# Optimization experiments

Measured on AMD Instinct MI355X. Metric: run time of the kernel, lower is better.

Reference implementation:

```python
import jax, jax.numpy as jnp
import numpy as np

NUM_HEAD = 12
D_MODEL = 768
SEQ_LEN = 4096
D_K = D_MODEL // NUM_HEAD
NEG = -1e9  # matches masked_fill(-1000000000.0)


def setup_inputs() -> dict:
    key = jax.random.key(0)
    ks = jax.random.split(key, 9)
    s = 1.0 / np.sqrt(D_MODEL)
    inp = {
        "x": jax.random.normal(ks[0], (1, SEQ_LEN, D_MODEL), jnp.float32),
        "Wq": jax.random.normal(ks[1], (D_MODEL, D_MODEL), jnp.float32) * s,
        "bq": jax.random.normal(ks[2], (D_MODEL,), jnp.float32) * 0.01,
        "Wk": jax.random.normal(ks[3], (D_MODEL, D_MODEL), jnp.float32) * s,
        "bk": jax.random.normal(ks[4], (D_MODEL,), jnp.float32) * 0.01,
        "Wv": jax.random.normal(ks[5], (D_MODEL, D_MODEL), jnp.float32) * s,
        "bv": jax.random.normal(ks[6], (D_MODEL,), jnp.float32) * 0.01,
        "Wo": jax.random.normal(ks[7], (D_MODEL, D_MODEL), jnp.float32) * s,
        "bo": jax.random.normal(ks[8], (D_MODEL,), jnp.float32) * 0.01,
    }
    return inp


def reference(x, Wq, bq, Wk, bk, Wv, bv, Wo, bo):
    # x: [B, S, D]. nn.Linear computes x @ W.T + b.
    B, S, D = x.shape

    def proj(W, b):
        y = jnp.einsum("bsd,ed->bse", x, W) + b
        # [B, S, H, d_k] -> [B, H, S, d_k]
        return y.reshape(B, S, NUM_HEAD, D_K).transpose(0, 2, 1, 3)

    q = proj(Wq, bq)
    k = proj(Wk, bk)
    v = proj(Wv, bv)

    scores = jnp.einsum("bhqd,bhkd->bhqk", q, k) / jnp.sqrt(
        jnp.asarray(D_K, x.dtype)
    )
    # causal (subsequent) mask: position q attends to k <= q
    causal = jnp.tril(jnp.ones((S, S), bool))
    scores = jnp.where(causal[None, None], scores, jnp.asarray(NEG, x.dtype))
    p_attn = jax.nn.softmax(scores, axis=-1)  # dropout is identity in eval
    ctx = jnp.einsum("bhqk,bhkd->bhqd", p_attn, v)
    ctx = ctx.transpose(0, 2, 1, 3).reshape(B, S, D)
    return jnp.einsum("bsd,ed->bse", ctx, Wo) + bo
```

## Files before the change

### kernel.cpp

```cpp
#include <hip/hip_runtime.h>

#define SEQ 4096
#define DM  768
#define NH  12
#define DK  64

typedef __bf16 bf16_t;
typedef bf16_t bf16x8 __attribute__((ext_vector_type(8)));
typedef bf16_t bf16x4 __attribute__((ext_vector_type(4)));
typedef float  f32x4  __attribute__((ext_vector_type(4)));
typedef short  s16x4  __attribute__((ext_vector_type(4)));

#define LOG2E 1.44269504088896340736f
#define SM_C  16.0f

static __device__ inline f32x4 mfma16x16x16_bf16(bf16x4 a, bf16x4 b, f32x4 c) {
#if __has_builtin(__builtin_amdgcn_mfma_f32_16x16x16_bf16)
    return __builtin_amdgcn_mfma_f32_16x16x16_bf16(a, b, c, 0, 0, 0);
#else
    return __builtin_amdgcn_mfma_f32_16x16x16bf16_1k(
        __builtin_bit_cast(s16x4, a), __builtin_bit_cast(s16x4, b), c, 0, 0, 0);
#endif
}

static __device__ __forceinline__ void gl_lds16(const bf16_t* g, bf16_t* l) {
    __builtin_amdgcn_global_load_lds(
        (const __attribute__((address_space(1))) void*)g,
        (__attribute__((address_space(3))) void*)l, 16, 0, 0);
}

__global__ __launch_bounds__(256) void cvt_zero(
    const float* __restrict__ x,  const float* __restrict__ Wq,
    const float* __restrict__ Wk, const float* __restrict__ Wv,
    const float* __restrict__ Wo,
    bf16_t* __restrict__ xb, bf16_t* __restrict__ Wb,
    float* __restrict__ zf )
{
    const int NXV  = SEQ * DM / 4;
    const int NWV  = DM * DM / 4;
    const int NCVT = NXV + 4 * NWV;
    int i4 = blockIdx.x * 256 + threadIdx.x;
    if (i4 < NCVT) {
        const float* src; bf16_t* dst; int off;
        if (i4 < NXV) { src = x; dst = xb; off = i4; }
        else {
            int j = i4 - NXV;
            int w = j / NWV, jj = j - w * NWV;
            src = (w == 0) ? Wq : (w == 1) ? Wk : (w == 2) ? Wv : Wo;
            dst = Wb + (size_t)w * DM * DM;
            off = jj;
        }
        float4 v = *(const float4*)&src[(size_t)off * 4];
        bf16x4 t;
        t[0] = (bf16_t)v.x; t[1] = (bf16_t)v.y;
        t[2] = (bf16_t)v.z; t[3] = (bf16_t)v.w;
        *(bf16x4*)&dst[(size_t)off * 4] = t;
    } else {
        int j = i4 - NCVT;
        *(float4*)&zf[(size_t)j * 4] = (float4){0.f, 0.f, 0.f, 0.f};
    }
}

__global__ __launch_bounds__(256) void gemm_qkv2(
    const bf16_t* __restrict__ A, const bf16_t* __restrict__ Wb,
    const float* __restrict__ bq, const float* __restrict__ bk,
    const float* __restrict__ bv,
    bf16_t* __restrict__ Qb, bf16_t* __restrict__ Kb, bf16_t* __restrict__ Vbt)
{
    const int z = blockIdx.z;
    const bf16_t* W = Wb + (size_t)z * DM * DM;
    const float* bias = (z == 0) ? bq : (z == 1) ? bk : bv;

    __shared__ bf16_t As[128][64];
    __shared__ bf16_t Bs[128][64];

    const int tid  = threadIdx.x;
    const int wave = tid >> 6;
    const int lane = tid & 63;
    const int wm   = wave & 1, wn = wave >> 1;
    const int lrow = lane & 15;
    const int quad = lane >> 4;
    const int row0 = blockIdx.x * 128;
    const int col0 = blockIdx.y * 128;

    const int srow   = lane >> 3;
    const int schunk = (lane & 7) ^ srow;
    const int swz    = lrow & 7;

    f32x4 acc[4][4];
    #pragma unroll
    for (int i = 0; i < 4; i++)
        #pragma unroll
        for (int j = 0; j < 4; j++)
            acc[i][j] = (f32x4){0.f, 0.f, 0.f, 0.f};

    for (int k0 = 0; k0 < DM; k0 += 64) {
        __syncthreads();
        #pragma unroll
        for (int u = 0; u < 4; u++) {
            int R0 = wave * 32 + u * 8;
            gl_lds16(&A[(size_t)(row0 + R0 + srow) * DM + k0 + schunk * 8],
                     &As[R0][0]);
            gl_lds16(&W[(size_t)(col0 + R0 + srow) * DM + k0 + schunk * 8],
                     &Bs[R0][0]);
        }
        __syncthreads();

        #pragma unroll
        for (int s = 0; s < 2; s++) {
            bf16x8 af[4], bfr[4];
            #pragma unroll
            for (int mt = 0; mt < 4; mt++)
                af[mt] = *(const bf16x8*)
                    &As[wm * 64 + mt * 16 + lrow][(((s << 2) | quad) ^ swz) * 8];
            #pragma unroll
            for (int nt = 0; nt < 4; nt++)
                bfr[nt] = *(const bf16x8*)
                    &Bs[wn * 64 + nt * 16 + lrow][(((s << 2) | quad) ^ swz) * 8];
            #pragma unroll
            for (int mt = 0; mt < 4; mt++)
                #pragma unroll
                for (int nt = 0; nt < 4; nt++)
                    acc[mt][nt] = __builtin_amdgcn_mfma_f32_16x16x32_bf16(
                        af[mt], bfr[nt], acc[mt][nt], 0, 0, 0);
        }
    }

    if (z == 2) {
        #pragma unroll
        for (int nt = 0; nt < 4; nt++) {
            int col = col0 + wn * 64 + nt * 16 + lrow;
            float bvv = bias[col];
            #pragma unroll
            for (int mt = 0; mt < 4; mt++) {
                int row = row0 + wm * 64 + mt * 16 + quad * 4;
                bf16x4 t;
                #pragma unroll
                for (int r = 0; r < 4; r++) t[r] = (bf16_t)(acc[mt][nt][r] + bvv);
                *(bf16x4*)&Vbt[(size_t)col * SEQ + row] = t;
            }
        }
    } else {
        bf16_t* Cout = (z == 0) ? Qb : Kb;
        float scale = (z == 1) ? 0.125f : 1.0f;
        #pragma unroll
        for (int nt = 0; nt < 4; nt++) {
            int col = col0 + wn * 64 + nt * 16 + lrow;
            float bvv = bias[col];
            #pragma unroll
            for (int mt = 0; mt < 4; mt++) {
                #pragma unroll
                for (int r = 0; r < 4; r++) {
                    int row = row0 + wm * 64 + mt * 16 + quad * 4 + r;
                    Cout[(size_t)row * DM + col] =
                        (bf16_t)((acc[mt][nt][r] + bvv) * scale);
                }
            }
        }
    }
}

__global__ __launch_bounds__(256) void gemm_out2(
    const bf16_t* __restrict__ A, const bf16_t* __restrict__ W,
    const float* __restrict__ bias, float* __restrict__ C)
{
    __shared__ bf16_t As[128][64];
    __shared__ bf16_t Bs[64][64];

    const int tid  = threadIdx.x;
    const int wave = tid >> 6;
    const int lane = tid & 63;
    const int wm   = wave & 1, wn = wave >> 1;
    const int lrow = lane & 15;
    const int quad = lane >> 4;
    const int row0 = blockIdx.x * 128;
    const int col0 = blockIdx.y * 64;

    const int srow   = lane >> 3;
    const int schunk = (lane & 7) ^ srow;
    const int swz    = lrow & 7;

    f32x4 acc[4][2];
    #pragma unroll
    for (int i = 0; i < 4; i++)
        #pragma unroll
        for (int j = 0; j < 2; j++)
            acc[i][j] = (f32x4){0.f, 0.f, 0.f, 0.f};

    for (int k0 = 0; k0 < DM; k0 += 64) {
        __syncthreads();
        #pragma unroll
        for (int u = 0; u < 4; u++) {
            int R0 = wave * 32 + u * 8;
            gl_lds16(&A[(size_t)(row0 + R0 + srow) * DM + k0 + schunk * 8],
                     &As[R0][0]);
        }
        #pragma unroll
        for (int u = 0; u < 2; u++) {
            int R0 = wave * 16 + u * 8;
            gl_lds16(&W[(size_t)(col0 + R0 + srow) * DM + k0 + schunk * 8],
                     &Bs[R0][0]);
        }
        __syncthreads();

        #pragma unroll
        for (int s = 0; s < 2; s++) {
            bf16x8 af[4], bfr[2];
            #pragma unroll
            for (int mt = 0; mt < 4; mt++)
                af[mt] = *(const bf16x8*)
                    &As[wm * 64 + mt * 16 + lrow][(((s << 2) | quad) ^ swz) * 8];
            #pragma unroll
            for (int nt = 0; nt < 2; nt++)
                bfr[nt] = *(const bf16x8*)
                    &Bs[wn * 32 + nt * 16 + lrow][(((s << 2) | quad) ^ swz) * 8];
            #pragma unroll
            for (int mt = 0; mt < 4; mt++)
                #pragma unroll
                for (int nt = 0; nt < 2; nt++)
                    acc[mt][nt] = __builtin_amdgcn_mfma_f32_16x16x32_bf16(
                        af[mt], bfr[nt], acc[mt][nt], 0, 0, 0);
        }
    }

    #pragma unroll
    for (int nt = 0; nt < 2; nt++) {
        int col = col0 + wn * 32 + nt * 16 + lrow;
        float bvv = bias[col];
        #pragma unroll
        for (int mt = 0; mt < 4; mt++) {
            #pragma unroll
            for (int r = 0; r < 4; r++) {
                int row = row0 + wm * 64 + mt * 16 + quad * 4 + r;
                C[(size_t)row * DM + col] = acc[mt][nt][r] + bvv;
            }
        }
    }
}

__global__ __launch_bounds__(256) void flash_q128(
    const bf16_t* __restrict__ Qb, const bf16_t* __restrict__ Kb,
    const bf16_t* __restrict__ Vbt,
    float* __restrict__ Oacc ,
    float* __restrict__ Lacc )
{
    const int qi     = blockIdx.x;
    const int s0     = blockIdx.y * 16;
    const int lastkt = 2 * qi + 1;
    if (s0 > lastkt) return;
    const int h    = blockIdx.z;
    const int kend = min(s0 + 15, lastkt);
    const int tid  = threadIdx.x;
    const int wave = tid >> 6;
    const int lane = tid & 63;
    const int lrow = lane & 15;
    const int quad = lane >> 4;

    __shared__ bf16_t Ks[2][64][72];
    __shared__ bf16_t Vt[2][64][76];

    bf16x8 qfrag[2][2];
    #pragma unroll
    for (int g = 0; g < 2; g++) {
        size_t qr = (size_t)(qi * 128 + g * 64 + wave * 16 + lrow) * DM + h * DK;
        qfrag[g][0] = *(const bf16x8*)&Qb[qr + quad * 8];
        qfrag[g][1] = *(const bf16x8*)&Qb[qr + 32 + quad * 8];
    }

    f32x4 oT[2][4];
    #pragma unroll
    for (int g = 0; g < 2; g++)
        #pragma unroll
        for (int dt = 0; dt < 4; dt++) oT[g][dt] = (f32x4){0.f, 0.f, 0.f, 0.f};
    float l_i[2] = {0.f, 0.f};

    const int r0 = tid >> 3;
    const int c0 = (tid & 7) * 8;
    const bf16_t* Kbase = Kb  + (size_t)h * DK + c0;
    const bf16_t* Vbase = Vbt + (size_t)(h * DK) * SEQ + c0;

    size_t ko = (size_t)s0 * 64;
    bf16x8 kr0 = *(const bf16x8*)&Kbase[(ko + r0)      * DM];
    bf16x8 kr1 = *(const bf16x8*)&Kbase[(ko + r0 + 32) * DM];
    bf16x8 vr0 = *(const bf16x8*)&Vbase[(size_t)(r0)      * SEQ + ko];
    bf16x8 vr1 = *(const bf16x8*)&Vbase[(size_t)(r0 + 32) * SEQ + ko];

    for (int kt = s0; kt <= kend; kt++) {
        const int b = kt & 1;
        *(bf16x8*)&Ks[b][r0][c0]      = kr0;
        *(bf16x8*)&Ks[b][r0 + 32][c0] = kr1;
        *(bf16x8*)&Vt[b][r0][c0]      = vr0;
        *(bf16x8*)&Vt[b][r0 + 32][c0] = vr1;
        __syncthreads();

        if (kt < kend) {
            size_t kn = (size_t)(kt + 1) * 64;
            kr0 = *(const bf16x8*)&Kbase[(kn + r0)      * DM];
            kr1 = *(const bf16x8*)&Kbase[(kn + r0 + 32) * DM];
            vr0 = *(const bf16x8*)&Vbase[(size_t)(r0)      * SEQ + kn];
            vr1 = *(const bf16x8*)&Vbase[(size_t)(r0 + 32) * SEQ + kn];
        }

        #pragma unroll
        for (int g = 0; g < 2; g++) {
            if (kt > 2 * qi + g) continue;

            f32x4 sc[4];
            #pragma unroll
            for (int mt = 0; mt < 4; mt++) {
                f32x4 a = (f32x4){0.f, 0.f, 0.f, 0.f};
                #pragma unroll
                for (int s = 0; s < 2; s++) {
                    bf16x8 kf = *(const bf16x8*)&Ks[b][mt * 16 + lrow][s * 32 + quad * 8];
                    a = __builtin_amdgcn_mfma_f32_16x16x32_bf16(
                        kf, qfrag[g][s], a, 0, 0, 0);
                }
                sc[mt] = a;
            }

            if (kt == 2 * qi + g) {
                int lqr = qi * 128 + g * 64 + wave * 16 + lrow - kt * 64;
                #pragma unroll
                for (int mt = 0; mt < 4; mt++)
                    #pragma unroll
                    for (int r = 0; r < 4; r++)
                        if (mt * 16 + quad * 4 + r > lqr) sc[mt][r] = -1e30f;
            }

            bf16x4 pf[4];
            float rsum = 0.f;
            #pragma unroll
            for (int mt = 0; mt < 4; mt++) {
                bf16x4 t;
                #pragma unroll
                for (int r = 0; r < 4; r++) {
                    float p = __builtin_amdgcn_exp2f(
                        __builtin_fmaf(sc[mt][r], LOG2E, -SM_C * LOG2E));
                    rsum += p;
                    t[r] = (bf16_t)p;
                }
                pf[mt] = t;
            }
            l_i[g] += rsum;

            #pragma unroll
            for (int dt = 0; dt < 4; dt++)
                #pragma unroll
                for (int kb = 0; kb < 4; kb++) {
                    bf16x4 vf = *(const bf16x4*)&Vt[b][dt * 16 + lrow][kb * 16 + quad * 4];
                    oT[g][dt] = mfma16x16x16_bf16(vf, pf[kb], oT[g][dt]);
                }
        }
    }

    #pragma unroll
    for (int g = 0; g < 2; g++) {
        int q0g = qi * 128 + g * 64;
        #pragma unroll
        for (int dt = 0; dt < 4; dt++)
            #pragma unroll
            for (int r = 0; r < 4; r++) {
                int d = dt * 16 + quad * 4 + r;
                atomicAdd(&Oacc[((size_t)h * DK + d) * SEQ + q0g + wave * 16 + lrow],
                          oT[g][dt][r]);
            }
        float ls = l_i[g];
        ls += __shfl_xor(ls, 16, 64);
        ls += __shfl_xor(ls, 32, 64);
        if (quad == 0)
            atomicAdd(&Lacc[(size_t)h * SEQ + q0g + wave * 16 + lrow], ls);
    }
}

__global__ __launch_bounds__(256) void ctx_epilogue(
    const float* __restrict__ Oacc, const float* __restrict__ Lacc,
    bf16_t* __restrict__ Ctx)
{
    const int qt = blockIdx.x;
    const int h  = blockIdx.y;
    const int tid = threadIdx.x;
    __shared__ float T[64][65];

    #pragma unroll
    for (int i = 0; i < 4; i++) {
        int v  = tid + i * 256;
        int d  = v >> 4;
        int qv = v & 15;
        f32x4 o4 = *(const f32x4*)&Oacc[((size_t)h * DK + d) * SEQ + qt * 64 + qv * 4];
        f32x4 l4 = *(const f32x4*)&Lacc[(size_t)h * SEQ + qt * 64 + qv * 4];
        #pragma unroll
        for (int j = 0; j < 4; j++)
            T[qv * 4 + j][d] = o4[j] / l4[j];
    }
    __syncthreads();
    #pragma unroll
    for (int i = 0; i < 2; i++) {
        int v  = tid + i * 256;
        int q  = v >> 3;
        int c8 = v & 7;
        bf16x8 t;
        #pragma unroll
        for (int j = 0; j < 8; j++)
            t[j] = (bf16_t)T[q][c8 * 8 + j];
        *(bf16x8*)&Ctx[(size_t)(qt * 64 + q) * DM + h * DK + c8 * 8] = t;
    }
}

extern "C" void kernel_launch(void* const* d_in, const int* in_sizes, int n_in,
                              void* d_out, int out_size, void* d_ws, size_t ws_size,
                              hipStream_t stream) {
    const float* x  = (const float*)d_in[0];
    const float* Wq = (const float*)d_in[1];
    const float* bq = (const float*)d_in[2];
    const float* Wk = (const float*)d_in[3];
    const float* bk = (const float*)d_in[4];
    const float* Wv = (const float*)d_in[5];
    const float* bv = (const float*)d_in[6];
    const float* Wo = (const float*)d_in[7];
    const float* bo = (const float*)d_in[8];
    float* out = (float*)d_out;

    const size_t NX = (size_t)SEQ * DM;
    const size_t NW = (size_t)DM * DM;

    bf16_t* xb   = (bf16_t*)d_ws;
    bf16_t* Qb   = xb  + NX;
    bf16_t* Kb   = Qb  + NX;
    bf16_t* Vbt  = Kb  + NX;
    bf16_t* Wb   = Vbt + NX;
    float*  Oacc = (float*)(Wb + 4 * NW);
    float*  Lacc = Oacc + NX;
    bf16_t* Cx   = xb;

    int total_blocks = (1376256 + 798720) / 256;
    cvt_zero<<<total_blocks, 256, 0, stream>>>(x, Wq, Wk, Wv, Wo, xb, Wb, Oacc);

    dim3 g1(SEQ / 128, DM / 128, 3);
    gemm_qkv2<<<g1, 256, 0, stream>>>(xb, Wb, bq, bk, bv, Qb, Kb, Vbt);

    dim3 g2(SEQ / 128, 4, NH);
    flash_q128<<<g2, 256, 0, stream>>>(Qb, Kb, Vbt, Oacc, Lacc);

    dim3 g3(SEQ / 64, NH);
    ctx_epilogue<<<g3, 256, 0, stream>>>(Oacc, Lacc, Cx);

    dim3 g4(SEQ / 128, DM / 64);
    gemm_out2<<<g4, 256, 0, stream>>>(Cx, Wb + 3 * NW, bo, out);
}
```

Baseline: 212.9 us.

## Replace LDS-staged flash kernel with per-wave register-streamed, sync-free attention

Rewrites the attention kernel so each wave owns two 16-row query tiles and streams 16-key K/V fragments straight from global memory into registers, with a one-step prefetch. This removes the shared-memory staging and the __syncthreads barriers. The key dimension is split into 512-wide chunks (8 per query tile instead of 4 of 1024), with partial results merged through atomics. The tradeoff is more redundant global/L2 traffic, since every wave reloads K/V itself, plus more atomic adds. In return it gets finer causal skipping and launch bounds that target higher occupancy.

```diff
diff --git a/kernel.cpp b/kernel.cpp
--- a/kernel.cpp
+++ b/kernel.cpp
@@ -34,7 +34,7 @@
     const float* __restrict__ Wk, const float* __restrict__ Wv,
     const float* __restrict__ Wo,
     bf16_t* __restrict__ xb, bf16_t* __restrict__ Wb,
-    float* __restrict__ zf )
+    float* __restrict__ zf)
 {
     const int NXV  = SEQ * DM / 4;
     const int NWV  = DM * DM / 4;
@@ -238,137 +238,139 @@
     }
 }
 
-__global__ __launch_bounds__(256) void flash_q128(
+__global__ __launch_bounds__(256, 4) void flash_nosync(
     const bf16_t* __restrict__ Qb, const bf16_t* __restrict__ Kb,
     const bf16_t* __restrict__ Vbt,
     float* __restrict__ Oacc ,
     float* __restrict__ Lacc )
 {
-    const int qi     = blockIdx.x;
-    const int s0     = blockIdx.y * 16;
-    const int lastkt = 2 * qi + 1;
-    if (s0 > lastkt) return;
+    const int qt = blockIdx.x;
+    const int kc = blockIdx.y;
+    if (kc * 512 > qt * 128 + 127) return;
     const int h    = blockIdx.z;
-    const int kend = min(s0 + 15, lastkt);
     const int tid  = threadIdx.x;
     const int wave = tid >> 6;
     const int lane = tid & 63;
     const int lrow = lane & 15;
     const int quad = lane >> 4;
 
-    __shared__ bf16_t Ks[2][64][72];
-    __shared__ bf16_t Vt[2][64][76];
-
-    bf16x8 qfrag[2][2];
-    #pragma unroll
-    for (int g = 0; g < 2; g++) {
-        size_t qr = (size_t)(qi * 128 + g * 64 + wave * 16 + lrow) * DM + h * DK;
-        qfrag[g][0] = *(const bf16x8*)&Qb[qr + quad * 8];
-        qfrag[g][1] = *(const bf16x8*)&Qb[qr + 32 + quad * 8];
-    }
-
-    f32x4 oT[2][4];
-    #pragma unroll
-    for (int g = 0; g < 2; g++)
-        #pragma unroll
-        for (int dt = 0; dt < 4; dt++) oT[g][dt] = (f32x4){0.f, 0.f, 0.f, 0.f};
-    float l_i[2] = {0.f, 0.f};
-
-    const int r0 = tid >> 3;
-    const int c0 = (tid & 7) * 8;
-    const bf16_t* Kbase = Kb  + (size_t)h * DK + c0;
-    const bf16_t* Vbase = Vbt + (size_t)(h * DK) * SEQ + c0;
-
-    size_t ko = (size_t)s0 * 64;
-    bf16x8 kr0 = *(const bf16x8*)&Kbase[(ko + r0)      * DM];
-    bf16x8 kr1 = *(const bf16x8*)&Kbase[(ko + r0 + 32) * DM];
-    bf16x8 vr0 = *(const bf16x8*)&Vbase[(size_t)(r0)      * SEQ + ko];
-    bf16x8 vr1 = *(const bf16x8*)&Vbase[(size_t)(r0 + 32) * SEQ + ko];
-
-    for (int kt = s0; kt <= kend; kt++) {
-        const int b = kt & 1;
-        *(bf16x8*)&Ks[b][r0][c0]      = kr0;
-        *(bf16x8*)&Ks[b][r0 + 32][c0] = kr1;
-        *(bf16x8*)&Vt[b][r0][c0]      = vr0;
-        *(bf16x8*)&Vt[b][r0 + 32][c0] = vr1;
-        __syncthreads();
-
-        if (kt < kend) {
-            size_t kn = (size_t)(kt + 1) * 64;
-            kr0 = *(const bf16x8*)&Kbase[(kn + r0)      * DM];
-            kr1 = *(const bf16x8*)&Kbase[(kn + r0 + 32) * DM];
-            vr0 = *(const bf16x8*)&Vbase[(size_t)(r0)      * SEQ + kn];
-            vr1 = *(const bf16x8*)&Vbase[(size_t)(r0 + 32) * SEQ + kn];
-        }
-
-        #pragma unroll
-        for (int g = 0; g < 2; g++) {
-            if (kt > 2 * qi + g) continue;
-
-            f32x4 sc[4];
-            #pragma unroll
-            for (int mt = 0; mt < 4; mt++) {
-                f32x4 a = (f32x4){0.f, 0.f, 0.f, 0.f};
-                #pragma unroll
-                for (int s = 0; s < 2; s++) {
-                    bf16x8 kf = *(const bf16x8*)&Ks[b][mt * 16 + lrow][s * 32 + quad * 8];
-                    a = __builtin_amdgcn_mfma_f32_16x16x32_bf16(
-                        kf, qfrag[g][s], a, 0, 0, 0);
-                }
-                sc[mt] = a;
-            }
-
-            if (kt == 2 * qi + g) {
-                int lqr = qi * 128 + g * 64 + wave * 16 + lrow - kt * 64;
-                #pragma unroll
-                for (int mt = 0; mt < 4; mt++)
-                    #pragma unroll
-                    for (int r = 0; r < 4; r++)
-                        if (mt * 16 + quad * 4 + r > lqr) sc[mt][r] = -1e30f;
-            }
-
-            bf16x4 pf[4];
+    const int ma = 8 * qt + 2 * wave;
+    const int mb = ma + 1;
+    const int ktbeg = kc * 32;
+    const int ktend = min(kc * 32 + 31, mb);
+    if (ktbeg > ktend) return;
+
+    size_t qra = (size_t)(ma * 16 + lrow) * DM + h * DK;
+    size_t qrb = qra + (size_t)16 * DM;
+    bf16x8 qa0 = *(const bf16x8*)&Qb[qra + quad * 8];
+    bf16x8 qa1 = *(const bf16x8*)&Qb[qra + 32 + quad * 8];
+    bf16x8 qb0 = *(const bf16x8*)&Qb[qrb + quad * 8];
+    bf16x8 qb1 = *(const bf16x8*)&Qb[qrb + 32 + quad * 8];
+
+    f32x4 oa[4], ob[4];
+    #pragma unroll
+    for (int dt = 0; dt < 4; dt++) {
+        oa[dt] = (f32x4){0.f, 0.f, 0.f, 0.f};
+        ob[dt] = (f32x4){0.f, 0.f, 0.f, 0.f};
+    }
+    float la = 0.f, lb = 0.f;
+
+    const bf16_t* Kp = Kb  + (size_t)h * DK;
+    const bf16_t* Vp = Vbt + (size_t)(h * DK) * SEQ;
+
+    bf16x8 kf0, kf1;
+    bf16x4 vf0, vf1, vf2, vf3;
+    {
+        int kb = ktbeg * 16;
+        const bf16_t* kr = Kp + (size_t)(kb + lrow) * DM + quad * 8;
+        kf0 = *(const bf16x8*)kr;
+        kf1 = *(const bf16x8*)(kr + 32);
+        vf0 = *(const bf16x4*)&Vp[(size_t)(lrow)      * SEQ + kb + quad * 4];
+        vf1 = *(const bf16x4*)&Vp[(size_t)(16 + lrow) * SEQ + kb + quad * 4];
+        vf2 = *(const bf16x4*)&Vp[(size_t)(32 + lrow) * SEQ + kb + quad * 4];
+        vf3 = *(const bf16x4*)&Vp[(size_t)(48 + lrow) * SEQ + kb + quad * 4];
+    }
+
+    for (int kt = ktbeg; kt <= ktend; kt++) {
+        bf16x8 ck0 = kf0, ck1 = kf1;
+        bf16x4 cv0 = vf0, cv1 = vf1, cv2 = vf2, cv3 = vf3;
+        if (kt < ktend) {
+            int kb = (kt + 1) * 16;
+            const bf16_t* kr = Kp + (size_t)(kb + lrow) * DM + quad * 8;
+            kf0 = *(const bf16x8*)kr;
+            kf1 = *(const bf16x8*)(kr + 32);
+            vf0 = *(const bf16x4*)&Vp[(size_t)(lrow)      * SEQ + kb + quad * 4];
+            vf1 = *(const bf16x4*)&Vp[(size_t)(16 + lrow) * SEQ + kb + quad * 4];
+            vf2 = *(const bf16x4*)&Vp[(size_t)(32 + lrow) * SEQ + kb + quad * 4];
+            vf3 = *(const bf16x4*)&Vp[(size_t)(48 + lrow) * SEQ + kb + quad * 4];
+        }
+
+        {
+            f32x4 a = (f32x4){0.f, 0.f, 0.f, 0.f};
+            a = __builtin_amdgcn_mfma_f32_16x16x32_bf16(ck0, qb0, a, 0, 0, 0);
+            a = __builtin_amdgcn_mfma_f32_16x16x32_bf16(ck1, qb1, a, 0, 0, 0);
+            if (kt == mb) {
+                #pragma unroll
+                for (int r = 0; r < 4; r++)
+                    if (quad * 4 + r > lrow) a[r] = -1e30f;
+            }
+            bf16x4 pf;
             float rsum = 0.f;
             #pragma unroll
-            for (int mt = 0; mt < 4; mt++) {
-                bf16x4 t;
-                #pragma unroll
-                for (int r = 0; r < 4; r++) {
-                    float p = __builtin_amdgcn_exp2f(
-                        __builtin_fmaf(sc[mt][r], LOG2E, -SM_C * LOG2E));
-                    rsum += p;
-                    t[r] = (bf16_t)p;
-                }
-                pf[mt] = t;
-            }
-            l_i[g] += rsum;
-
-            #pragma unroll
-            for (int dt = 0; dt < 4; dt++)
-                #pragma unroll
-                for (int kb = 0; kb < 4; kb++) {
-                    bf16x4 vf = *(const bf16x4*)&Vt[b][dt * 16 + lrow][kb * 16 + quad * 4];
-                    oT[g][dt] = mfma16x16x16_bf16(vf, pf[kb], oT[g][dt]);
-                }
-        }
-    }
-
-    #pragma unroll
-    for (int g = 0; g < 2; g++) {
-        int q0g = qi * 128 + g * 64;
-        #pragma unroll
-        for (int dt = 0; dt < 4; dt++)
-            #pragma unroll
             for (int r = 0; r < 4; r++) {
-                int d = dt * 16 + quad * 4 + r;
-                atomicAdd(&Oacc[((size_t)h * DK + d) * SEQ + q0g + wave * 16 + lrow],
-                          oT[g][dt][r]);
-            }
-        float ls = l_i[g];
-        ls += __shfl_xor(ls, 16, 64);
-        ls += __shfl_xor(ls, 32, 64);
-        if (quad == 0)
-            atomicAdd(&Lacc[(size_t)h * SEQ + q0g + wave * 16 + lrow], ls);
+                float p = __builtin_amdgcn_exp2f(
+                    __builtin_fmaf(a[r], LOG2E, -SM_C * LOG2E));
+                rsum += p;
+                pf[r] = (bf16_t)p;
+            }
+            lb += rsum;
+            ob[0] = mfma16x16x16_bf16(cv0, pf, ob[0]);
+            ob[1] = mfma16x16x16_bf16(cv1, pf, ob[1]);
+            ob[2] = mfma16x16x16_bf16(cv2, pf, ob[2]);
+            ob[3] = mfma16x16x16_bf16(cv3, pf, ob[3]);
+        }
+
+        if (kt <= ma) {
+            f32x4 a = (f32x4){0.f, 0.f, 0.f, 0.f};
+            a = __builtin_amdgcn_mfma_f32_16x16x32_bf16(ck0, qa0, a, 0, 0, 0);
+            a = __builtin_amdgcn_mfma_f32_16x16x32_bf16(ck1, qa1, a, 0, 0, 0);
+            if (kt == ma) {
+                #pragma unroll
+                for (int r = 0; r < 4; r++)
+                    if (quad * 4 + r > lrow) a[r] = -1e30f;
+            }
+            bf16x4 pf;
+            float rsum = 0.f;
+            #pragma unroll
+            for (int r = 0; r < 4; r++) {
+                float p = __builtin_amdgcn_exp2f(
+                    __builtin_fmaf(a[r], LOG2E, -SM_C * LOG2E));
+                rsum += p;
+                pf[r] = (bf16_t)p;
+            }
+            la += rsum;
+            oa[0] = mfma16x16x16_bf16(cv0, pf, oa[0]);
+            oa[1] = mfma16x16x16_bf16(cv1, pf, oa[1]);
+            oa[2] = mfma16x16x16_bf16(cv2, pf, oa[2]);
+            oa[3] = mfma16x16x16_bf16(cv3, pf, oa[3]);
+        }
+    }
+
+    #pragma unroll
+    for (int dt = 0; dt < 4; dt++)
+        #pragma unroll
+        for (int r = 0; r < 4; r++) {
+            int d = dt * 16 + quad * 4 + r;
+            atomicAdd(&Oacc[((size_t)h * DK + d) * SEQ + ma * 16 + lrow], oa[dt][r]);
+            atomicAdd(&Oacc[((size_t)h * DK + d) * SEQ + mb * 16 + lrow], ob[dt][r]);
+        }
+    la += __shfl_xor(la, 16, 64);
+    la += __shfl_xor(la, 32, 64);
+    lb += __shfl_xor(lb, 16, 64);
+    lb += __shfl_xor(lb, 32, 64);
+    if (quad == 0) {
+        atomicAdd(&Lacc[(size_t)h * SEQ + ma * 16 + lrow], la);
+        atomicAdd(&Lacc[(size_t)h * SEQ + mb * 16 + lrow], lb);
     }
 }
 
@@ -438,8 +440,8 @@
     dim3 g1(SEQ / 128, DM / 128, 3);
     gemm_qkv2<<<g1, 256, 0, stream>>>(xb, Wb, bq, bk, bv, Qb, Kb, Vbt);
 
-    dim3 g2(SEQ / 128, 4, NH);
-    flash_q128<<<g2, 256, 0, stream>>>(Qb, Kb, Vbt, Oacc, Lacc);
+    dim3 g2(SEQ / 128, SEQ / 512, NH);
+    flash_nosync<<<g2, 256, 0, stream>>>(Qb, Kb, Vbt, Oacc, Lacc);
 
     dim3 g3(SEQ / 64, NH);
     ctx_epilogue<<<g3, 256, 0, stream>>>(Oacc, Lacc, Cx);
```

After: 397.4 us. 1.87x slower.
